# Kernel optimization log

Hardware: AMD Instinct MI355X
Metric: run time of the kernel (lower is better)

## Reference

```python
import jax, jax.numpy as jnp
import numpy as np

S, B, T, I, H, O = 8, 32, 512, 256, 512, 32


def setup_inputs() -> dict:
    key = jax.random.key(0)
    ks = jax.random.split(key, 8)
    x = jax.random.normal(ks[0], (S, B, T, I), dtype=jnp.float32)
    lengths = jax.random.randint(ks[1], (S,), T // 2, T + 1, dtype=jnp.int32)
    s = 1.0 / np.sqrt(H)
    u = lambda k, shp: jax.random.uniform(k, shp, jnp.float32, -s, s)
    return {
        'x': x,
        'lengths': lengths,
        'W_ih': u(ks[2], (3 * H, I)),
        'W_hh': u(ks[3], (3 * H, H)),
        'b_ih': u(ks[4], (3 * H,)),
        'b_hh': u(ks[5], (3 * H,)),
        'W_out': u(ks[6], (O, H)),
        'b_out': u(ks[7], (O,)),
    }


def reference(x, lengths, W_ih, W_hh, b_ih, b_hh, W_out, b_out):
    # x: [S, B, T, I] padded ragged batch; lengths: [S] valid steps per sequence.
    # Precompute input projections for all gates in one big GEMM: [S, B, T, 3H]
    xW = jnp.einsum('sbti,gi->sbtg', x, W_ih) + b_ih

    def run_seq(xw, length):
        # xw: [B, T, 3H]; one ragged 'sequence' (a mini-batch in the original list)
        def step(h, inp):
            xw_t, t = inp  # xw_t: [B, 3H]
            hW = h @ W_hh.T + b_hh
            xr, xz, xn = jnp.split(xw_t, 3, axis=-1)
            hr, hz, hn = jnp.split(hW, 3, axis=-1)
            r = jax.nn.sigmoid(xr + hr)
            z = jax.nn.sigmoid(xz + hz)
            n = jnp.tanh(xn + r * hn)
            h_new = (1.0 - z) * n + z * h
            # freeze hidden state past the valid length -> h ends at step length-1
            h = jnp.where(t < length, h_new, h)
            return h, None

        h0 = jnp.zeros((B, H), dtype=xw.dtype)
        hT, _ = jax.lax.scan(step, h0, (jnp.swapaxes(xw, 0, 1), jnp.arange(T)))
        return hT.mean(axis=0)  # output[:, -1].mean(0) -> [H]

    hbar = jax.vmap(run_seq)(xW, lengths)  # [S, H]
    return hbar @ W_out.T + b_out  # [S, O]
```

## Files before the change

### kernel.cpp

```cpp
#include <hip/hip_runtime.h>
#include <hip/hip_bf16.h>

#define S_ 8
#define B_ 32
#define T_ 512
#define I_ 256
#define H_ 512
#define O_ 32

typedef __attribute__((ext_vector_type(8))) short short8;
typedef __attribute__((ext_vector_type(4))) float float4_;

__device__ inline unsigned short f2bf(float f) {
    unsigned u = __float_as_uint(f);
    u = (u + 0x7fffu + ((u >> 16) & 1u)) >> 16;
    return (unsigned short)u;
}

__device__ inline short8 load_cvt8(const float* p) {
    float4_ a = *reinterpret_cast<const float4_*>(p);
    float4_ b = *reinterpret_cast<const float4_*>(p + 4);
    short8 r;
    r[0] = (short)f2bf(a[0]); r[1] = (short)f2bf(a[1]);
    r[2] = (short)f2bf(a[2]); r[3] = (short)f2bf(a[3]);
    r[4] = (short)f2bf(b[0]); r[5] = (short)f2bf(b[1]);
    r[6] = (short)f2bf(b[2]); r[7] = (short)f2bf(b[3]);
    return r;
}

__device__ inline short8 load_h16_coherent(const unsigned short* p) {
    short8 v;
    asm volatile("global_load_dwordx4 %0, %1, off sc0 sc1"
                 : "=v"(v) : "v"(p) : "memory");
    return v;
}
__device__ inline unsigned load_u32_coherent(const unsigned* p) {
    unsigned v;
    asm volatile("global_load_dword %0, %1, off sc0 sc1"
                 : "=v"(v) : "v"(p) : "memory");
    return v;
}
__device__ inline void store_h16_coherent(unsigned short* p, short8 v) {
    asm volatile("global_store_dwordx4 %0, %1, off sc0 sc1"
                 :: "v"(p), "v"(v) : "memory");
}
__device__ inline void store_u32_coherent(unsigned* p, unsigned v) {
    asm volatile("global_store_dword %0, %1, off sc0 sc1"
                 :: "v"(p), "v"(v) : "memory");
}
__device__ inline void wait_vm0_fence() {
    asm volatile("s_waitcnt vmcnt(0)" ::: "memory");
    __builtin_amdgcn_sched_barrier(0);
}
__device__ inline void wait_lgkm0_fence() {
    asm volatile("s_waitcnt lgkmcnt(0)" ::: "memory");
    __builtin_amdgcn_sched_barrier(0);
}

#define WS_NEED 546816

__global__ __launch_bounds__(256, 1)
void zgru_persistent(const float* __restrict__ x, const int* __restrict__ lens,
                     const float* __restrict__ Wih, const float* __restrict__ Whh,
                     const float* __restrict__ bih, const float* __restrict__ bhh,
                     const float* __restrict__ Wout, const float* __restrict__ bout,
                     float* __restrict__ out,
                     unsigned short* __restrict__ hbuf, float* __restrict__ hbar,
                     unsigned* __restrict__ flags, unsigned* __restrict__ done_ctr)
{
    const int tid  = threadIdx.x;
    const int wg   = blockIdx.x;
    const int s    = wg & 7;
    const int j    = wg >> 3;
    const int wid  = tid >> 6;
    const int lane = tid & 63;
    const int m    = wid >> 1;
    const int kh   = wid & 1;
    const int lrow = lane & 15;
    const int lgrp = lane >> 4;

    const int len = lens[s];

    __shared__ unsigned short whh_lds[48 * 512];
    __shared__ float4_ xch[2][4][64];
    __shared__ unsigned short hsh[2][16 * 24];
    __shared__ unsigned fxch[2];
    __shared__ unsigned last_flag;
    __shared__ float red[8][32];

    for (int gi = tid; gi < 48 * 64; gi += 256) {
        const int blk = gi >> 6, ln = gi & 63;
        const int khb = blk / 24, rem = blk % 24;
        const int g = rem >> 3, kc = rem & 7;
        const int lg = ln >> 4, lc = ln & 15;
        const float* src = Whh + (size_t)(g * H_ + 16 * j + lc) * H_
                         + 256 * khb + 32 * kc + 8 * lg;
        *reinterpret_cast<short8*>(&whh_lds[(size_t)blk * 512 + ln * 8]) = load_cvt8(src);
    }
    if (tid < 2) fxch[tid] = 0;

    short8 bxR[4], bxZ[4], bxN[4];
    {
        const int gr = 16 * j + lrow;
        #pragma unroll
        for (int kc = 0; kc < 4; ++kc) {
            const int k0 = 128 * kh + 32 * kc + 8 * lgrp;
            bxR[kc] = load_cvt8(Wih + (size_t)(gr          ) * I_ + k0);
            bxZ[kc] = load_cvt8(Wih + (size_t)(gr +     H_ ) * I_ + k0);
            bxN[kc] = load_cvt8(Wih + (size_t)(gr + 2 * H_ ) * I_ + k0);
        }
    }

    const int gcol   = 16 * j + lrow;
    const float bsR  = bih[gcol] + bhh[gcol];
    const float bsZ  = bih[H_ + gcol] + bhh[H_ + gcol];
    const float biN  = bih[2 * H_ + gcol];
    const float bhN_ = bhh[2 * H_ + gcol];

    __syncthreads();

    short8 bh[24];
    #pragma unroll
    for (int q = 0; q < 24; ++q)
        bh[q] = *reinterpret_cast<const short8*>(&whh_lds[(size_t)(kh * 24 + q) * 512 + lane * 8]);

    float h[4] = {0.f, 0.f, 0.f, 0.f};

    const size_t HBUF = (size_t)S_ * B_ * H_;
    const int arow = 16 * m + lrow;
    const unsigned* fg = flags + (size_t)(s * 2 + m) * 64;
    unsigned* myflag   = flags + (size_t)(s * 2 + m) * 64 + j;

    for (int t = 0; t < len; ++t) {
        float4_ aR = {0,0,0,0}, aZ = {0,0,0,0}, aNX = {0,0,0,0};
        {
            const float* xb = x + (((size_t)s * B_ + arow) * T_ + t) * I_ + 128 * kh + 8 * lgrp;
            #pragma unroll
            for (int kc = 0; kc < 4; ++kc) {
                short8 ax = load_cvt8(xb + 32 * kc);
                aR  = __builtin_amdgcn_mfma_f32_16x16x32_bf16(ax, bxR[kc], aR, 0, 0, 0);
                aZ  = __builtin_amdgcn_mfma_f32_16x16x32_bf16(ax, bxZ[kc], aZ, 0, 0, 0);
                aNX = __builtin_amdgcn_mfma_f32_16x16x32_bf16(ax, bxN[kc], aNX, 0, 0, 0);
            }
        }

        if (t > 0) {
            const unsigned tgt = (unsigned)t;
            for (;;) {
                unsigned fv = load_u32_coherent(fg + (lane & 31));
                asm volatile("s_waitcnt vmcnt(0)" ::: "memory");
                if (__ballot(fv >= tgt) == ~0ull) break;
            }
            __builtin_amdgcn_sched_barrier(0);
        }

        const unsigned short* hr = hbuf + (size_t)(t & 1) * HBUF + (size_t)s * B_ * H_;
        short8 ah[8];
        #pragma unroll
        for (int kc = 0; kc < 8; ++kc)
            ah[kc] = load_h16_coherent(hr + (size_t)arow * H_ + 256 * kh + 32 * kc + 8 * lgrp);
        wait_vm0_fence();

        float4_ aNH = {0,0,0,0};
        #pragma unroll
        for (int kc = 0; kc < 8; ++kc) {
            aR  = __builtin_amdgcn_mfma_f32_16x16x32_bf16(ah[kc], bh[kc     ], aR,  0, 0, 0);
            aZ  = __builtin_amdgcn_mfma_f32_16x16x32_bf16(ah[kc], bh[kc +  8], aZ,  0, 0, 0);
            aNH = __builtin_amdgcn_mfma_f32_16x16x32_bf16(ah[kc], bh[kc + 16], aNH, 0, 0, 0);
        }

        if (kh == 1) {
            xch[m][0][lane] = aR;
            xch[m][1][lane] = aZ;
            xch[m][2][lane] = aNH;
            xch[m][3][lane] = aNX;
            __hip_atomic_store(&fxch[m], (unsigned)(t + 1),
                               __ATOMIC_RELEASE, __HIP_MEMORY_SCOPE_WORKGROUP);
        } else {
            while (__hip_atomic_load(&fxch[m], __ATOMIC_ACQUIRE, __HIP_MEMORY_SCOPE_WORKGROUP)
                   < (unsigned)(t + 1)) {}
            __builtin_amdgcn_sched_barrier(0);
            aR  += xch[m][0][lane];
            aZ  += xch[m][1][lane];
            aNH += xch[m][2][lane];
            aNX += xch[m][3][lane];

            unsigned short* hs = &hsh[m][0];
            #pragma unroll
            for (int i = 0; i < 4; ++i) {
                const float pr = aR[i] + bsR;
                const float pz = aZ[i] + bsZ;
                const float r = 1.f / (1.f + __expf(-pr));
                const float z = 1.f / (1.f + __expf(-pz));
                const float pn = aNX[i] + biN + r * (aNH[i] + bhN_);
                const float e = __expf(-2.f * fabsf(pn));
                float n = (1.f - e) / (1.f + e);
                n = copysignf(n, pn);
                h[i] = z * (h[i] - n) + n;
                hs[(4 * lgrp + i) * 24 + lrow] = f2bf(h[i]);
            }
            wait_lgkm0_fence();
            unsigned short* hw = hbuf + (size_t)((t + 1) & 1) * HBUF + (size_t)s * B_ * H_;
            if (lane < 32) {
                const int row = lane >> 1, cc = lane & 1;
                short8 v = *reinterpret_cast<const short8*>(&hs[row * 24 + cc * 8]);
                store_h16_coherent(hw + (size_t)(16 * m + row) * H_ + 16 * j + cc * 8, v);
            }
            asm volatile("s_waitcnt vmcnt(0)" ::: "memory");
            if (lane == 0)
                store_u32_coherent(myflag, (unsigned)(t + 1));
        }
    }

    float s4 = h[0] + h[1] + h[2] + h[3];
    s4 += __shfl_xor(s4, 16);
    s4 += __shfl_xor(s4, 32);
    if (kh == 0 && lgrp == 0)
        atomicAdd(&hbar[(size_t)s * H_ + gcol], s4);

    __syncthreads();
    if (tid == 0) {
        unsigned old = __hip_atomic_fetch_add(&done_ctr[s * 64], 1u,
                                              __ATOMIC_RELAXED, __HIP_MEMORY_SCOPE_AGENT);
        last_flag = (old == 31u) ? 1u : 0u;
    }
    __syncthreads();
    if (last_flag) {
        const int o = tid & 31;
        const int p = tid >> 5;
        float acc = 0.f;
        const float* hb = hbar + (size_t)s * H_;
        const float* wr = Wout + (size_t)o * H_;
        for (int hh = 64 * p; hh < 64 * p + 64; ++hh) {
            float hv = __hip_atomic_load(&hb[hh], __ATOMIC_RELAXED, __HIP_MEMORY_SCOPE_AGENT);
            acc += hv * wr[hh];
        }
        red[p][o] = acc;
        __syncthreads();
        if (tid < 32) {
            float v = 0.f;
            #pragma unroll
            for (int q = 0; q < 8; ++q) v += red[q][tid];
            out[s * O_ + tid] = v * (1.f / 32.f) + bout[tid];
        }
    }
}

extern "C" void kernel_launch(void* const* d_in, const int* in_sizes, int n_in,
                              void* d_out, int out_size, void* d_ws, size_t ws_size,
                              hipStream_t stream) {
    (void)in_sizes; (void)n_in; (void)out_size; (void)ws_size;
    const float* x    = (const float*)d_in[0];
    const int*   lens = (const int*)d_in[1];
    const float* Wih  = (const float*)d_in[2];
    const float* Whh  = (const float*)d_in[3];
    const float* bih  = (const float*)d_in[4];
    const float* bhh  = (const float*)d_in[5];
    const float* Wout = (const float*)d_in[6];
    const float* bout = (const float*)d_in[7];
    float* out = (float*)d_out;

    char* wsc = (char*)d_ws;
    unsigned short* hbuf = (unsigned short*)wsc;
    float*    hbar  = (float*)(wsc + 524288);
    unsigned* flags = (unsigned*)(wsc + 540672);
    unsigned* dctr  = (unsigned*)(wsc + 544768);

    hipMemsetAsync(d_ws, 0, WS_NEED, stream);

    zgru_persistent<<<dim3(256), dim3(256), 0, stream>>>(
        x, lens, Wih, Whh, bih, bhh, Wout, bout, out, hbuf, hbar, flags, dctr);
}
```

Before: 1.963 ms.

## Replace flag-based step sync with tagged fp32 hidden-state polling and prefetch x

Removes the separate per-step flag array. Each hidden value is now stored as fp32 with the step tag packed into its two low mantissa bits, and consumers poll the hidden-state buffer directly until every tag matches. This drops one round trip (store h, wait, store flag, then poll flag and load h) from the serial recurrence. The next step's x row is also prefetched into registers during the current step, and W_hh fragments are read from LDS per step instead of being held in registers. In exchange the h buffer doubles in size, each poll loads more data, h loses two mantissa bits, and the spin loops are now bounded by iteration caps.

```diff
diff --git a/kernel.cpp b/kernel.cpp
--- a/kernel.cpp
+++ b/kernel.cpp
@@ -11,53 +11,35 @@
 typedef __attribute__((ext_vector_type(8))) short short8;
 typedef __attribute__((ext_vector_type(4))) float float4_;
 
-__device__ inline unsigned short f2bf(float f) {
+__device__ __forceinline__ unsigned short f2bf(float f) {
     unsigned u = __float_as_uint(f);
     u = (u + 0x7fffu + ((u >> 16) & 1u)) >> 16;
     return (unsigned short)u;
 }
-
-__device__ inline short8 load_cvt8(const float* p) {
-    float4_ a = *reinterpret_cast<const float4_*>(p);
-    float4_ b = *reinterpret_cast<const float4_*>(p + 4);
+__device__ __forceinline__ short8 cvt2(float4_ a, float4_ b) {
     short8 r;
-    r[0] = (short)f2bf(a[0]); r[1] = (short)f2bf(a[1]);
-    r[2] = (short)f2bf(a[2]); r[3] = (short)f2bf(a[3]);
-    r[4] = (short)f2bf(b[0]); r[5] = (short)f2bf(b[1]);
-    r[6] = (short)f2bf(b[2]); r[7] = (short)f2bf(b[3]);
+    r[0]=(short)f2bf(a[0]); r[1]=(short)f2bf(a[1]); r[2]=(short)f2bf(a[2]); r[3]=(short)f2bf(a[3]);
+    r[4]=(short)f2bf(b[0]); r[5]=(short)f2bf(b[1]); r[6]=(short)f2bf(b[2]); r[7]=(short)f2bf(b[3]);
     return r;
 }
-
-__device__ inline short8 load_h16_coherent(const unsigned short* p) {
-    short8 v;
-    asm volatile("global_load_dwordx4 %0, %1, off sc0 sc1"
-                 : "=v"(v) : "v"(p) : "memory");
+__device__ __forceinline__ short8 load_cvt8(const float* p) {
+    return cvt2(*reinterpret_cast<const float4_*>(p), *reinterpret_cast<const float4_*>(p + 4));
+}
+
+__device__ __forceinline__ float4_ ld16f(const float* p) {
+    float4_ v;
+    asm volatile("global_load_dwordx4 %0, %1, off sc0 sc1" : "=v"(v) : "v"(p) : "memory");
     return v;
 }
-__device__ inline unsigned load_u32_coherent(const unsigned* p) {
-    unsigned v;
-    asm volatile("global_load_dword %0, %1, off sc0 sc1"
-                 : "=v"(v) : "v"(p) : "memory");
-    return v;
-}
-__device__ inline void store_h16_coherent(unsigned short* p, short8 v) {
-    asm volatile("global_store_dwordx4 %0, %1, off sc0 sc1"
-                 :: "v"(p), "v"(v) : "memory");
-}
-__device__ inline void store_u32_coherent(unsigned* p, unsigned v) {
-    asm volatile("global_store_dword %0, %1, off sc0 sc1"
-                 :: "v"(p), "v"(v) : "memory");
-}
-__device__ inline void wait_vm0_fence() {
+__device__ __forceinline__ void st16f(float* p, float4_ v) {
+    asm volatile("global_store_dwordx4 %0, %1, off sc0 sc1" :: "v"(p), "v"(v) : "memory");
+}
+__device__ __forceinline__ void vm0() {
     asm volatile("s_waitcnt vmcnt(0)" ::: "memory");
     __builtin_amdgcn_sched_barrier(0);
 }
-__device__ inline void wait_lgkm0_fence() {
-    asm volatile("s_waitcnt lgkmcnt(0)" ::: "memory");
-    __builtin_amdgcn_sched_barrier(0);
-}
-
-#define WS_NEED 546816
+
+#define WS_NEED 1067008
 
 __global__ __launch_bounds__(256, 1)
 void zgru_persistent(const float* __restrict__ x, const int* __restrict__ lens,
@@ -65,8 +47,8 @@
                      const float* __restrict__ bih, const float* __restrict__ bhh,
                      const float* __restrict__ Wout, const float* __restrict__ bout,
                      float* __restrict__ out,
-                     unsigned short* __restrict__ hbuf, float* __restrict__ hbar,
-                     unsigned* __restrict__ flags, unsigned* __restrict__ done_ctr)
+                     float* __restrict__ hbufF, float* __restrict__ hbar,
+                     unsigned* __restrict__ done_ctr)
 {
     const int tid  = threadIdx.x;
     const int wg   = blockIdx.x;
@@ -83,7 +65,7 @@
 
     __shared__ unsigned short whh_lds[48 * 512];
     __shared__ float4_ xch[2][4][64];
-    __shared__ unsigned short hsh[2][16 * 24];
+    __shared__ float hshF[2][16][16];
     __shared__ unsigned fxch[2];
     __shared__ unsigned last_flag;
     __shared__ float red[8][32];
@@ -119,54 +101,77 @@
 
     __syncthreads();
 
-    short8 bh[24];
-    #pragma unroll
-    for (int q = 0; q < 24; ++q)
-        bh[q] = *reinterpret_cast<const short8*>(&whh_lds[(size_t)(kh * 24 + q) * 512 + lane * 8]);
-
     float h[4] = {0.f, 0.f, 0.f, 0.f};
 
-    const size_t HBUF = (size_t)S_ * B_ * H_;
+    const size_t HBUFF = (size_t)S_ * B_ * H_;
     const int arow = 16 * m + lrow;
-    const unsigned* fg = flags + (size_t)(s * 2 + m) * 64;
-    unsigned* myflag   = flags + (size_t)(s * 2 + m) * 64 + j;
+    const float* xlane = x + ((size_t)s * B_ + arow) * T_ * I_ + 128 * kh + 8 * lgrp;
+    const float* hrF0  = hbufF + ((size_t)s * B_ + arow) * H_ + 256 * kh + 8 * lgrp;
+    float*       hwF0  = hbufF + ((size_t)s * B_ + 16 * m) * H_ + 16 * j;
+
+    float4_ xraw[8];
+    {
+        const float* xp = xlane;
+        #pragma unroll
+        for (int kc = 0; kc < 4; ++kc) {
+            xraw[2*kc]   = *reinterpret_cast<const float4_*>(xp + 32*kc);
+            xraw[2*kc+1] = *reinterpret_cast<const float4_*>(xp + 32*kc + 4);
+        }
+    }
 
     for (int t = 0; t < len; ++t) {
+        short8 ax[4];
+        #pragma unroll
+        for (int kc = 0; kc < 4; ++kc) ax[kc] = cvt2(xraw[2*kc], xraw[2*kc+1]);
         float4_ aR = {0,0,0,0}, aZ = {0,0,0,0}, aNX = {0,0,0,0};
+        #pragma unroll
+        for (int kc = 0; kc < 4; ++kc) {
+            aR  = __builtin_amdgcn_mfma_f32_16x16x32_bf16(ax[kc], bxR[kc], aR, 0, 0, 0);
+            aZ  = __builtin_amdgcn_mfma_f32_16x16x32_bf16(ax[kc], bxZ[kc], aZ, 0, 0, 0);
+            aNX = __builtin_amdgcn_mfma_f32_16x16x32_bf16(ax[kc], bxN[kc], aNX, 0, 0, 0);
+        }
+
+        const float* hrF = hrF0 + (size_t)(t & 1) * HBUFF;
+        const unsigned tag = (unsigned)t & 3u;
+        float4_ hraw[16];
+        for (int it = 0; it < (1 << 19); ++it) {
+            #pragma unroll
+            for (int kc = 0; kc < 8; ++kc) {
+                hraw[2*kc]   = ld16f(hrF + 32 * kc);
+                hraw[2*kc+1] = ld16f(hrF + 32 * kc + 4);
+            }
+            vm0();
+            unsigned acc = 0;
+            #pragma unroll
+            for (int q = 0; q < 16; ++q)
+                #pragma unroll
+                for (int e = 0; e < 4; ++e)
+                    acc |= (__float_as_uint(hraw[q][e]) ^ tag);
+            if (__ballot((acc & 3u) == 0u) == ~0ull) break;
+        }
+
         {
-            const float* xb = x + (((size_t)s * B_ + arow) * T_ + t) * I_ + 128 * kh + 8 * lgrp;
+            const int tn = (t + 1 < len) ? (t + 1) : t;
+            const float* xp = xlane + (size_t)tn * I_;
             #pragma unroll
             for (int kc = 0; kc < 4; ++kc) {
-                short8 ax = load_cvt8(xb + 32 * kc);
-                aR  = __builtin_amdgcn_mfma_f32_16x16x32_bf16(ax, bxR[kc], aR, 0, 0, 0);
-                aZ  = __builtin_amdgcn_mfma_f32_16x16x32_bf16(ax, bxZ[kc], aZ, 0, 0, 0);
-                aNX = __builtin_amdgcn_mfma_f32_16x16x32_bf16(ax, bxN[kc], aNX, 0, 0, 0);
-            }
-        }
-
-        if (t > 0) {
-            const unsigned tgt = (unsigned)t;
-            for (;;) {
-                unsigned fv = load_u32_coherent(fg + (lane & 31));
-                asm volatile("s_waitcnt vmcnt(0)" ::: "memory");
-                if (__ballot(fv >= tgt) == ~0ull) break;
-            }
-            __builtin_amdgcn_sched_barrier(0);
-        }
-
-        const unsigned short* hr = hbuf + (size_t)(t & 1) * HBUF + (size_t)s * B_ * H_;
+                xraw[2*kc]   = *reinterpret_cast<const float4_*>(xp + 32*kc);
+                xraw[2*kc+1] = *reinterpret_cast<const float4_*>(xp + 32*kc + 4);
+            }
+        }
+
         short8 ah[8];
         #pragma unroll
-        for (int kc = 0; kc < 8; ++kc)
-            ah[kc] = load_h16_coherent(hr + (size_t)arow * H_ + 256 * kh + 32 * kc + 8 * lgrp);
-        wait_vm0_fence();
-
+        for (int kc = 0; kc < 8; ++kc) ah[kc] = cvt2(hraw[2*kc], hraw[2*kc+1]);
         float4_ aNH = {0,0,0,0};
         #pragma unroll
         for (int kc = 0; kc < 8; ++kc) {
-            aR  = __builtin_amdgcn_mfma_f32_16x16x32_bf16(ah[kc], bh[kc     ], aR,  0, 0, 0);
-            aZ  = __builtin_amdgcn_mfma_f32_16x16x32_bf16(ah[kc], bh[kc +  8], aZ,  0, 0, 0);
-            aNH = __builtin_amdgcn_mfma_f32_16x16x32_bf16(ah[kc], bh[kc + 16], aNH, 0, 0, 0);
+            short8 bR = *reinterpret_cast<const short8*>(&whh_lds[(size_t)(kh*24 + kc     ) * 512 + lane * 8]);
+            short8 bZ = *reinterpret_cast<const short8*>(&whh_lds[(size_t)(kh*24 + kc +  8) * 512 + lane * 8]);
+            short8 bN = *reinterpret_cast<const short8*>(&whh_lds[(size_t)(kh*24 + kc + 16) * 512 + lane * 8]);
+            aR  = __builtin_amdgcn_mfma_f32_16x16x32_bf16(ah[kc], bR, aR,  0, 0, 0);
+            aZ  = __builtin_amdgcn_mfma_f32_16x16x32_bf16(ah[kc], bZ, aZ,  0, 0, 0);
+            aNH = __builtin_amdgcn_mfma_f32_16x16x32_bf16(ah[kc], bN, aNH, 0, 0, 0);
         }
 
         if (kh == 1) {
@@ -177,15 +182,17 @@
             __hip_atomic_store(&fxch[m], (unsigned)(t + 1),
                                __ATOMIC_RELEASE, __HIP_MEMORY_SCOPE_WORKGROUP);
         } else {
-            while (__hip_atomic_load(&fxch[m], __ATOMIC_ACQUIRE, __HIP_MEMORY_SCOPE_WORKGROUP)
-                   < (unsigned)(t + 1)) {}
+            for (int it = 0; it < (1 << 20); ++it) {
+                if (__hip_atomic_load(&fxch[m], __ATOMIC_ACQUIRE,
+                                      __HIP_MEMORY_SCOPE_WORKGROUP) >= (unsigned)(t + 1)) break;
+            }
             __builtin_amdgcn_sched_barrier(0);
             aR  += xch[m][0][lane];
             aZ  += xch[m][1][lane];
             aNH += xch[m][2][lane];
             aNX += xch[m][3][lane];
 
-            unsigned short* hs = &hsh[m][0];
+            const unsigned wtag = (unsigned)(t + 1) & 3u;
             #pragma unroll
             for (int i = 0; i < 4; ++i) {
                 const float pr = aR[i] + bsR;
@@ -197,18 +204,13 @@
                 float n = (1.f - e) / (1.f + e);
                 n = copysignf(n, pn);
                 h[i] = z * (h[i] - n) + n;
-                hs[(4 * lgrp + i) * 24 + lrow] = f2bf(h[i]);
-            }
-            wait_lgkm0_fence();
-            unsigned short* hw = hbuf + (size_t)((t + 1) & 1) * HBUF + (size_t)s * B_ * H_;
-            if (lane < 32) {
-                const int row = lane >> 1, cc = lane & 1;
-                short8 v = *reinterpret_cast<const short8*>(&hs[row * 24 + cc * 8]);
-                store_h16_coherent(hw + (size_t)(16 * m + row) * H_ + 16 * j + cc * 8, v);
-            }
-            asm volatile("s_waitcnt vmcnt(0)" ::: "memory");
-            if (lane == 0)
-                store_u32_coherent(myflag, (unsigned)(t + 1));
+                const unsigned u = (__float_as_uint(h[i]) & ~3u) | wtag;
+                hshF[m][4 * lgrp + i][lrow] = __uint_as_float(u);
+            }
+            float* hwF = hwF0 + (size_t)((t + 1) & 1) * HBUFF;
+            const int row = lane >> 2, c4 = (lane & 3) * 4;
+            float4_ v = *reinterpret_cast<const float4_*>(&hshF[m][row][c4]);
+            st16f(hwF + (size_t)row * H_ + c4, v);
         }
     }
 
@@ -261,13 +263,12 @@
     float* out = (float*)d_out;
 
     char* wsc = (char*)d_ws;
-    unsigned short* hbuf = (unsigned short*)wsc;
-    float*    hbar  = (float*)(wsc + 524288);
-    unsigned* flags = (unsigned*)(wsc + 540672);
-    unsigned* dctr  = (unsigned*)(wsc + 544768);
+    float*    hbufF = (float*)wsc;
+    float*    hbar  = (float*)(wsc + 1048576);
+    unsigned* dctr  = (unsigned*)(wsc + 1064960);
 
     hipMemsetAsync(d_ws, 0, WS_NEED, stream);
 
     zgru_persistent<<<dim3(256), dim3(256), 0, stream>>>(
-        x, lens, Wih, Whh, bih, bhh, Wout, bout, out, hbuf, hbar, flags, dctr);
-}
+        x, lens, Wih, Whh, bih, bhh, Wout, bout, out, hbufF, hbar, dctr);
+}
```

Result: slower. 3.943 ms (+100.8%).

## Prefetch next-step x rows and load recurrent weights directly into registers

Applied to the files above, without the earlier changes.

The x input for step t+1 is now loaded at the end of step t, so its global-load latency overlaps the wait on the cross-workgroup flag barrier instead of sitting on the critical path. W_hh is loaded straight from global into named registers, dropping the LDS staging buffer and the extra LDS read. Both spin loops now have iteration caps. A capped spin could exit early and read stale hidden state if another workgroup stalls for too long.

```diff
diff --git a/kernel.cpp b/kernel.cpp
--- a/kernel.cpp
+++ b/kernel.cpp
@@ -11,53 +11,45 @@
 typedef __attribute__((ext_vector_type(8))) short short8;
 typedef __attribute__((ext_vector_type(4))) float float4_;
 
-__device__ inline unsigned short f2bf(float f) {
+__device__ __forceinline__ unsigned short f2bf(float f) {
     unsigned u = __float_as_uint(f);
     u = (u + 0x7fffu + ((u >> 16) & 1u)) >> 16;
     return (unsigned short)u;
 }
-
-__device__ inline short8 load_cvt8(const float* p) {
-    float4_ a = *reinterpret_cast<const float4_*>(p);
-    float4_ b = *reinterpret_cast<const float4_*>(p + 4);
+__device__ __forceinline__ short8 cvt2(float4_ a, float4_ b) {
     short8 r;
-    r[0] = (short)f2bf(a[0]); r[1] = (short)f2bf(a[1]);
-    r[2] = (short)f2bf(a[2]); r[3] = (short)f2bf(a[3]);
-    r[4] = (short)f2bf(b[0]); r[5] = (short)f2bf(b[1]);
-    r[6] = (short)f2bf(b[2]); r[7] = (short)f2bf(b[3]);
+    r[0]=(short)f2bf(a[0]); r[1]=(short)f2bf(a[1]); r[2]=(short)f2bf(a[2]); r[3]=(short)f2bf(a[3]);
+    r[4]=(short)f2bf(b[0]); r[5]=(short)f2bf(b[1]); r[6]=(short)f2bf(b[2]); r[7]=(short)f2bf(b[3]);
     return r;
 }
-
-__device__ inline short8 load_h16_coherent(const unsigned short* p) {
+__device__ __forceinline__ short8 load_cvt8(const float* p) {
+    return cvt2(*reinterpret_cast<const float4_*>(p), *reinterpret_cast<const float4_*>(p + 4));
+}
+
+__device__ __forceinline__ short8 ld16c(const unsigned short* p) {
     short8 v;
-    asm volatile("global_load_dwordx4 %0, %1, off sc0 sc1"
-                 : "=v"(v) : "v"(p) : "memory");
+    asm volatile("global_load_dwordx4 %0, %1, off sc0 sc1" : "=v"(v) : "v"(p) : "memory");
     return v;
 }
-__device__ inline unsigned load_u32_coherent(const unsigned* p) {
+__device__ __forceinline__ unsigned ldu32c(const unsigned* p) {
     unsigned v;
-    asm volatile("global_load_dword %0, %1, off sc0 sc1"
-                 : "=v"(v) : "v"(p) : "memory");
+    asm volatile("global_load_dword %0, %1, off sc0 sc1" : "=v"(v) : "v"(p) : "memory");
     return v;
 }
-__device__ inline void store_h16_coherent(unsigned short* p, short8 v) {
-    asm volatile("global_store_dwordx4 %0, %1, off sc0 sc1"
-                 :: "v"(p), "v"(v) : "memory");
-}
-__device__ inline void store_u32_coherent(unsigned* p, unsigned v) {
-    asm volatile("global_store_dword %0, %1, off sc0 sc1"
-                 :: "v"(p), "v"(v) : "memory");
-}
-__device__ inline void wait_vm0_fence() {
+__device__ __forceinline__ void st16c(unsigned short* p, short8 v) {
+    asm volatile("global_store_dwordx4 %0, %1, off sc0 sc1" :: "v"(p), "v"(v) : "memory");
+}
+__device__ __forceinline__ void stu32c(unsigned* p, unsigned v) {
+    asm volatile("global_store_dword %0, %1, off sc0 sc1" :: "v"(p), "v"(v) : "memory");
+}
+__device__ __forceinline__ void vm0() {
     asm volatile("s_waitcnt vmcnt(0)" ::: "memory");
     __builtin_amdgcn_sched_barrier(0);
 }
-__device__ inline void wait_lgkm0_fence() {
-    asm volatile("s_waitcnt lgkmcnt(0)" ::: "memory");
-    __builtin_amdgcn_sched_barrier(0);
-}
 
 #define WS_NEED 546816
+
+#define MFMA_ __builtin_amdgcn_mfma_f32_16x16x32_bf16
 
 __global__ __launch_bounds__(256, 1)
 void zgru_persistent(const float* __restrict__ x, const int* __restrict__ lens,
@@ -81,35 +73,45 @@
 
     const int len = lens[s];
 
-    __shared__ unsigned short whh_lds[48 * 512];
     __shared__ float4_ xch[2][4][64];
-    __shared__ unsigned short hsh[2][16 * 24];
+    __shared__ __align__(16) unsigned short hsh[2][16 * 24];
     __shared__ unsigned fxch[2];
     __shared__ unsigned last_flag;
     __shared__ float red[8][32];
 
-    for (int gi = tid; gi < 48 * 64; gi += 256) {
-        const int blk = gi >> 6, ln = gi & 63;
-        const int khb = blk / 24, rem = blk % 24;
-        const int g = rem >> 3, kc = rem & 7;
-        const int lg = ln >> 4, lc = ln & 15;
-        const float* src = Whh + (size_t)(g * H_ + 16 * j + lc) * H_
-                         + 256 * khb + 32 * kc + 8 * lg;
-        *reinterpret_cast<short8*>(&whh_lds[(size_t)blk * 512 + ln * 8]) = load_cvt8(src);
-    }
     if (tid < 2) fxch[tid] = 0;
 
-    short8 bxR[4], bxZ[4], bxN[4];
-    {
-        const int gr = 16 * j + lrow;
-        #pragma unroll
-        for (int kc = 0; kc < 4; ++kc) {
-            const int k0 = 128 * kh + 32 * kc + 8 * lgrp;
-            bxR[kc] = load_cvt8(Wih + (size_t)(gr          ) * I_ + k0);
-            bxZ[kc] = load_cvt8(Wih + (size_t)(gr +     H_ ) * I_ + k0);
-            bxN[kc] = load_cvt8(Wih + (size_t)(gr + 2 * H_ ) * I_ + k0);
-        }
-    }
+    const int gr  = 16 * j + lrow;
+    const int khk = 256 * kh;
+    const int khi = 128 * kh;
+    const int lg8 = 8 * lgrp;
+
+    short8 bhR0,bhR1,bhR2,bhR3,bhR4,bhR5,bhR6,bhR7;
+    short8 bhZ0,bhZ1,bhZ2,bhZ3,bhZ4,bhZ5,bhZ6,bhZ7;
+    short8 bhN0,bhN1,bhN2,bhN3,bhN4,bhN5,bhN6,bhN7;
+    short8 bxR0,bxR1,bxR2,bxR3, bxZ0,bxZ1,bxZ2,bxZ3, bxN0,bxN1,bxN2,bxN3;
+
+#define LDBH(kc) \
+    bhR##kc = load_cvt8(Whh + (size_t)(gr          ) * H_ + khk + 32*kc + lg8); \
+    bhZ##kc = load_cvt8(Whh + (size_t)(gr +     H_ ) * H_ + khk + 32*kc + lg8); \
+    bhN##kc = load_cvt8(Whh + (size_t)(gr + 2 * H_ ) * H_ + khk + 32*kc + lg8);
+    LDBH(0) LDBH(1) LDBH(2) LDBH(3) LDBH(4) LDBH(5) LDBH(6) LDBH(7)
+#undef LDBH
+#define LDBX(kc) \
+    bxR##kc = load_cvt8(Wih + (size_t)(gr          ) * I_ + khi + 32*kc + lg8); \
+    bxZ##kc = load_cvt8(Wih + (size_t)(gr +     H_ ) * I_ + khi + 32*kc + lg8); \
+    bxN##kc = load_cvt8(Wih + (size_t)(gr + 2 * H_ ) * I_ + khi + 32*kc + lg8);
+    LDBX(0) LDBX(1) LDBX(2) LDBX(3)
+#undef LDBX
+    asm volatile("" : "+v"(bhR0),"+v"(bhR1),"+v"(bhR2),"+v"(bhR3),
+                      "+v"(bhR4),"+v"(bhR5),"+v"(bhR6),"+v"(bhR7));
+    asm volatile("" : "+v"(bhZ0),"+v"(bhZ1),"+v"(bhZ2),"+v"(bhZ3),
+                      "+v"(bhZ4),"+v"(bhZ5),"+v"(bhZ6),"+v"(bhZ7));
+    asm volatile("" : "+v"(bhN0),"+v"(bhN1),"+v"(bhN2),"+v"(bhN3),
+                      "+v"(bhN4),"+v"(bhN5),"+v"(bhN6),"+v"(bhN7));
+    asm volatile("" : "+v"(bxR0),"+v"(bxR1),"+v"(bxR2),"+v"(bxR3),
+                      "+v"(bxZ0),"+v"(bxZ1),"+v"(bxZ2),"+v"(bxZ3),
+                      "+v"(bxN0),"+v"(bxN1),"+v"(bxN2),"+v"(bxN3));
 
     const int gcol   = 16 * j + lrow;
     const float bsR  = bih[gcol] + bhh[gcol];
@@ -119,55 +121,60 @@
 
     __syncthreads();
 
-    short8 bh[24];
-    #pragma unroll
-    for (int q = 0; q < 24; ++q)
-        bh[q] = *reinterpret_cast<const short8*>(&whh_lds[(size_t)(kh * 24 + q) * 512 + lane * 8]);
-
     float h[4] = {0.f, 0.f, 0.f, 0.f};
 
     const size_t HBUF = (size_t)S_ * B_ * H_;
     const int arow = 16 * m + lrow;
-    const unsigned* fg = flags + (size_t)(s * 2 + m) * 64;
+    const float* xlane = x + ((size_t)s * B_ + arow) * T_ * I_ + khi + lg8;
+    const unsigned short* hrow = hbuf + ((size_t)s * B_ + arow) * H_ + khk + lg8;
+    unsigned short* hwrow = hbuf + ((size_t)s * B_ + 16 * m) * H_ + 16 * j;
+    const unsigned* fl = flags + (size_t)(s * 2 + m) * 64;
     unsigned* myflag   = flags + (size_t)(s * 2 + m) * 64 + j;
 
+    float4_ xq00,xq01,xq10,xq11,xq20,xq21,xq30,xq31;
+    {
+        const float* xp = xlane;
+#define LDXR(kc) \
+        xq##kc##0 = *reinterpret_cast<const float4_*>(xp + 32*kc); \
+        xq##kc##1 = *reinterpret_cast<const float4_*>(xp + 32*kc + 4);
+        LDXR(0) LDXR(1) LDXR(2) LDXR(3)
+#undef LDXR
+    }
+
     for (int t = 0; t < len; ++t) {
+        short8 ax0 = cvt2(xq00, xq01), ax1 = cvt2(xq10, xq11);
+        short8 ax2 = cvt2(xq20, xq21), ax3 = cvt2(xq30, xq31);
         float4_ aR = {0,0,0,0}, aZ = {0,0,0,0}, aNX = {0,0,0,0};
-        {
-            const float* xb = x + (((size_t)s * B_ + arow) * T_ + t) * I_ + 128 * kh + 8 * lgrp;
-            #pragma unroll
-            for (int kc = 0; kc < 4; ++kc) {
-                short8 ax = load_cvt8(xb + 32 * kc);
-                aR  = __builtin_amdgcn_mfma_f32_16x16x32_bf16(ax, bxR[kc], aR, 0, 0, 0);
-                aZ  = __builtin_amdgcn_mfma_f32_16x16x32_bf16(ax, bxZ[kc], aZ, 0, 0, 0);
-                aNX = __builtin_amdgcn_mfma_f32_16x16x32_bf16(ax, bxN[kc], aNX, 0, 0, 0);
-            }
-        }
+#define XMF(kc) \
+        aR  = MFMA_(ax##kc, bxR##kc, aR,  0, 0, 0); \
+        aZ  = MFMA_(ax##kc, bxZ##kc, aZ,  0, 0, 0); \
+        aNX = MFMA_(ax##kc, bxN##kc, aNX, 0, 0, 0);
+        XMF(0) XMF(1) XMF(2) XMF(3)
+#undef XMF
 
         if (t > 0) {
             const unsigned tgt = (unsigned)t;
-            for (;;) {
-                unsigned fv = load_u32_coherent(fg + (lane & 31));
-                asm volatile("s_waitcnt vmcnt(0)" ::: "memory");
+            for (int it = 0; it < (1 << 16); ++it) {
+                unsigned fv = ldu32c(fl + (lane & 31));
+                vm0();
                 if (__ballot(fv >= tgt) == ~0ull) break;
             }
-            __builtin_amdgcn_sched_barrier(0);
-        }
-
-        const unsigned short* hr = hbuf + (size_t)(t & 1) * HBUF + (size_t)s * B_ * H_;
-        short8 ah[8];
-        #pragma unroll
-        for (int kc = 0; kc < 8; ++kc)
-            ah[kc] = load_h16_coherent(hr + (size_t)arow * H_ + 256 * kh + 32 * kc + 8 * lgrp);
-        wait_vm0_fence();
+        }
+
+        const unsigned short* hr = hrow + (size_t)(t & 1) * HBUF;
+        short8 ah0,ah1,ah2,ah3,ah4,ah5,ah6,ah7;
+#define LDH(kc) ah##kc = ld16c(hr + 32*kc);
+        LDH(0) LDH(1) LDH(2) LDH(3) LDH(4) LDH(5) LDH(6) LDH(7)
+#undef LDH
+        vm0();
 
         float4_ aNH = {0,0,0,0};
-        #pragma unroll
-        for (int kc = 0; kc < 8; ++kc) {
-            aR  = __builtin_amdgcn_mfma_f32_16x16x32_bf16(ah[kc], bh[kc     ], aR,  0, 0, 0);
-            aZ  = __builtin_amdgcn_mfma_f32_16x16x32_bf16(ah[kc], bh[kc +  8], aZ,  0, 0, 0);
-            aNH = __builtin_amdgcn_mfma_f32_16x16x32_bf16(ah[kc], bh[kc + 16], aNH, 0, 0, 0);
-        }
+#define HMF(kc) \
+        aR  = MFMA_(ah##kc, bhR##kc, aR,  0, 0, 0); \
+        aZ  = MFMA_(ah##kc, bhZ##kc, aZ,  0, 0, 0); \
+        aNH = MFMA_(ah##kc, bhN##kc, aNH, 0, 0, 0);
+        HMF(0) HMF(1) HMF(2) HMF(3) HMF(4) HMF(5) HMF(6) HMF(7)
+#undef HMF
 
         if (kh == 1) {
             xch[m][0][lane] = aR;
@@ -177,8 +184,10 @@
             __hip_atomic_store(&fxch[m], (unsigned)(t + 1),
                                __ATOMIC_RELEASE, __HIP_MEMORY_SCOPE_WORKGROUP);
         } else {
-            while (__hip_atomic_load(&fxch[m], __ATOMIC_ACQUIRE, __HIP_MEMORY_SCOPE_WORKGROUP)
-                   < (unsigned)(t + 1)) {}
+            for (int it = 0; it < (1 << 20); ++it) {
+                if (__hip_atomic_load(&fxch[m], __ATOMIC_ACQUIRE,
+                                      __HIP_MEMORY_SCOPE_WORKGROUP) >= (unsigned)(t + 1)) break;
+            }
             __builtin_amdgcn_sched_barrier(0);
             aR  += xch[m][0][lane];
             aZ  += xch[m][1][lane];
@@ -199,16 +208,26 @@
                 h[i] = z * (h[i] - n) + n;
                 hs[(4 * lgrp + i) * 24 + lrow] = f2bf(h[i]);
             }
-            wait_lgkm0_fence();
-            unsigned short* hw = hbuf + (size_t)((t + 1) & 1) * HBUF + (size_t)s * B_ * H_;
+            asm volatile("s_waitcnt lgkmcnt(0)" ::: "memory");
+            __builtin_amdgcn_sched_barrier(0);
+            unsigned short* hw = hwrow + (size_t)((t + 1) & 1) * HBUF;
             if (lane < 32) {
                 const int row = lane >> 1, cc = lane & 1;
                 short8 v = *reinterpret_cast<const short8*>(&hs[row * 24 + cc * 8]);
-                store_h16_coherent(hw + (size_t)(16 * m + row) * H_ + 16 * j + cc * 8, v);
-            }
-            asm volatile("s_waitcnt vmcnt(0)" ::: "memory");
-            if (lane == 0)
-                store_u32_coherent(myflag, (unsigned)(t + 1));
+                st16c(hw + (size_t)row * H_ + cc * 8, v);
+            }
+            vm0();
+            if (lane == 0) stu32c(myflag, (unsigned)(t + 1));
+        }
+
+        {
+            const int tn = (t + 1 < len) ? (t + 1) : t;
+            const float* xp = xlane + (size_t)tn * I_;
+#define LDXR(kc) \
+            xq##kc##0 = *reinterpret_cast<const float4_*>(xp + 32*kc); \
+            xq##kc##1 = *reinterpret_cast<const float4_*>(xp + 32*kc + 4);
+            LDXR(0) LDXR(1) LDXR(2) LDXR(3)
+#undef LDXR
         }
     }
 
```

After: 2.517 ms. 28.2% more time.
